# Kernel tuning notes

Measured on AMD Instinct MI355X. Metric: run time of the kernel, lower is better.

The kernel has to match this reference:

```python
import jax, jax.numpy as jnp
import numpy as np
from jax import lax

DN = ('NHWC', 'HWIO', 'NHWC')

def hard_sigmoid(x):
    # Keras ConvLSTM2D default recurrent_activation
    return jnp.clip(0.2 * x + 0.5, 0.0, 1.0)

def conv2d_same(x, w):
    return lax.conv_general_dilated(x, w, (1, 1), 'SAME', dimension_numbers=DN)

def convlstm_layer(x, Wx, Wh, b):
    # x: [B,T,H,W,Cin]; Wx: [kh,kw,Cin,4F]; Wh: [kh,kw,F,4F]; b: [4F]
    B, T, H, W, Cin = x.shape
    F = Wh.shape[2]
    # Precompute input-to-gate convs for all timesteps in one big conv (same math).
    xg = conv2d_same(x.reshape(B * T, H, W, Cin), Wx).reshape(B, T, H, W, 4 * F) + b
    xg = jnp.moveaxis(xg, 1, 0)  # [T,B,H,W,4F]
    h0 = jnp.zeros((B, H, W, F), x.dtype)
    c0 = jnp.zeros((B, H, W, F), x.dtype)

    def step(carry, xg_t):
        h, c = carry
        gates = xg_t + conv2d_same(h, Wh)
        i, f, g, o = jnp.split(gates, 4, axis=-1)
        i = hard_sigmoid(i)
        f = hard_sigmoid(f)
        g = jnp.tanh(g)
        o = hard_sigmoid(o)
        c = f * c + i * g
        h = o * jnp.tanh(c)
        return (h, c), h

    (h, c), hs = lax.scan(step, (h0, c0), xg)
    outputs = jnp.moveaxis(hs, 0, 1)  # [B,T,H,W,F]
    return outputs, h, c

def setup_inputs() -> dict:
    key = jax.random.key(0)
    ks = jax.random.split(key, 8)
    B, T, H, W, Cin = 8, 10, 64, 64, 1
    F = 64
    k = 3
    sc = lambda fan: 1.0 / np.sqrt(fan)
    x = jax.random.normal(ks[0], (B, T, H, W, Cin), jnp.float32)
    Wx0 = jax.random.normal(ks[1], (k, k, Cin, 4 * F), jnp.float32) * sc(k * k * Cin)
    Wh0 = jax.random.normal(ks[2], (k, k, F, 4 * F), jnp.float32) * sc(k * k * F)
    b0 = jax.random.normal(ks[3], (4 * F,), jnp.float32) * 0.01
    Wx1 = jax.random.normal(ks[4], (k, k, F, 4 * F), jnp.float32) * sc(k * k * F)
    Wh1 = jax.random.normal(ks[5], (k, k, F, 4 * F), jnp.float32) * sc(k * k * F)
    b1 = jax.random.normal(ks[6], (4 * F,), jnp.float32) * 0.01
    return {'x': x, 'Wx0': Wx0, 'Wh0': Wh0, 'b0': b0, 'Wx1': Wx1, 'Wh1': Wh1, 'b1': b1}

def reference(x, Wx0, Wh0, b0, Wx1, Wh1, b1):
    out0, h0, c0 = convlstm_layer(x, Wx0, Wh0, b0)
    out1, h1, c1 = convlstm_layer(out0, Wx1, Wh1, b1)
    # Encoder returns per-layer [hidden_state, cell_state]; stack: [L,2,B,H,W,F]
    return jnp.stack([jnp.stack([h0, c0]), jnp.stack([h1, c1])])
```

## Files before the change

### kernel.cpp

```cpp
#include <hip/hip_runtime.h>


typedef __bf16 bf16x8 __attribute__((ext_vector_type(8)));
typedef float f32x4 __attribute__((ext_vector_type(4)));

#define BHWF (8 * 64 * 64 * 64)
#define TSTRIDE 72
#define NCELL 180

__device__ __forceinline__ float hsig(float x) {
    return fminf(fmaxf(fmaf(0.2f, x, 0.5f), 0.0f), 1.0f);
}

__device__ __forceinline__ float ftanh(float x) {
    float e = __expf(2.0f * x);
    return fmaf(-2.0f, __builtin_amdgcn_rcpf(e + 1.0f), 1.0f);
}

__device__ __forceinline__ ushort f2bf(float f) {
    unsigned u = __float_as_uint(f);
    return (ushort)((u + 0x7FFFu + ((u >> 16) & 1u)) >> 16);
}

__global__ void prep_w(const float* __restrict__ s0, const float* __restrict__ s1,
                       const float* __restrict__ s2, const float* __restrict__ wx0,
                       ushort* __restrict__ d0, ushort* __restrict__ d1,
                       ushort* __restrict__ d2, ushort* __restrict__ dx0) {
    int o = blockIdx.x * 256 + threadIdx.x;
    if (blockIdx.y == 3) {
        if (o < 8192) {
            int e    = o & 7;
            int lane = (o >> 3) & 63;
            int g    = (o >> 9) & 3;
            int fq   = (o >> 11) & 3;
            int k = (lane >> 4) * 8 + e;
            int n = g * 64 + fq * 16 + (lane & 15);
            dx0[o] = (k < 9) ? f2bf(wx0[k * 256 + n]) : (ushort)0;
        }
        return;
    }
    const float* s[3] = { s0, s1, s2 };
    ushort* d[3] = { d0, d1, d2 };
    int e    = o & 7;
    int lane = (o >> 3) & 63;
    int g    = (o >> 9) & 3;
    int fq   = (o >> 11) & 3;
    int kc   = (o >> 13) & 1;
    int tap  = o >> 14;
    int n = g * 64 + fq * 16 + (lane & 15);
    int k = tap * 64 + kc * 32 + (lane >> 4) * 8 + e;
    d[blockIdx.y][o] = f2bf(s[blockIdx.y][k * 256 + n]);
}

__device__ __forceinline__ void stage(const ushort* __restrict__ src,
                                      ushort* __restrict__ tile,
                                      int y0, int x0, int tid) {
    for (int v = tid; v < NCELL * 8; v += 256) {
        int cell = v >> 3, j = v & 7;
        int r = cell / 18, cc = cell - r * 18;
        int y = y0 - 1 + r, xx = x0 - 1 + cc;
        uint4 dv = make_uint4(0u, 0u, 0u, 0u);
        if ((unsigned)y < 64u && (unsigned)xx < 64u)
            dv = ((const uint4*)src)[(size_t)((y << 6) + xx) * 8 + j];
        *(uint4*)&tile[cell * TSTRIDE + j * 8] = dv;
    }
}

__device__ __forceinline__ void conv8(const ushort* __restrict__ tile,
                                      const ushort* __restrict__ WS,
                                      f32x4 (&acc)[8][4],
                                      int fq, int lane) {
    const int colA = lane & 15;
    const int quad = (lane >> 4) & 3;
    const ushort* wbase = WS + fq * 2048 + lane * 8;
    #pragma unroll
    for (int kc = 0; kc < 2; ++kc) {
        #pragma unroll
        for (int dx = 0; dx < 3; ++dx) {
            bf16x8 A[10];
            #pragma unroll
            for (int r = 0; r < 10; ++r)
                A[r] = *(const bf16x8*)&tile[(r * 18 + colA + dx) * TSTRIDE + kc * 32 + quad * 8];
            bf16x8 B[3][4];
            {
                const ushort* wp = wbase + (size_t)(dx * 2 + kc) * 8192;
                #pragma unroll
                for (int g = 0; g < 4; ++g) B[0][g] = *(const bf16x8*)&wp[g * 512];
            }
            #pragma unroll
            for (int dy = 0; dy < 3; ++dy) {
                if (dy < 2) {
                    const ushort* wp = wbase + (size_t)(((dy + 1) * 3 + dx) * 2 + kc) * 8192;
                    #pragma unroll
                    for (int g = 0; g < 4; ++g) B[dy + 1][g] = *(const bf16x8*)&wp[g * 512];
                }
                #pragma unroll
                for (int mt = 0; mt < 8; ++mt)
                    #pragma unroll
                    for (int g = 0; g < 4; ++g)
                        acc[mt][g] = __builtin_amdgcn_mfma_f32_16x16x32_bf16(
                            A[mt + dy], B[dy][g], acc[mt][g], 0, 0, 0);
            }
        }
    }
}

__global__ __launch_bounds__(256, 2) void step_merged(
    int l0_active, int l1_active, int last0, int last1,
    const float* __restrict__ x, const ushort* __restrict__ Wx0F,
    const ushort* __restrict__ Wh0S, const float* __restrict__ b0,
    const ushort* __restrict__ h0_prev, float* __restrict__ c0,
    ushort* __restrict__ h0_out, float* __restrict__ oh0, float* __restrict__ oc0,
    const ushort* __restrict__ xin, const ushort* __restrict__ Wx1S,
    const ushort* __restrict__ Wh1S, const float* __restrict__ b1,
    const ushort* __restrict__ h1_prev, float* __restrict__ c1,
    ushort* __restrict__ h1_out, float* __restrict__ oh1, float* __restrict__ oc1)
{
    __shared__ __align__(16) ushort tile1[NCELL * TSTRIDE];
    __shared__ __align__(16) ushort tile2[NCELL * TSTRIDE];
    __shared__ __align__(16) ushort xa[4096];

    const int z = blockIdx.z;
    bool isL1; int b;
    if (l0_active && l1_active) { isL1 = (z >= 8); b = z & 7; }
    else                        { isL1 = (l1_active != 0); b = z; }

    const int tid = threadIdx.x;
    const int lane = tid & 63;
    const int fq = tid >> 6;
    const int colA = lane & 15;
    const int quad = (lane >> 4) & 3;
    const int x0 = blockIdx.x * 16, y0 = blockIdx.y * 8;
    const int f = fq * 16 + colA;

    const ushort* h_prev = isL1 ? h1_prev : h0_prev;
    const float*  bias   = isL1 ? b1 : b0;
    float*        cbuf   = isL1 ? c1 : c0;
    ushort*       hout   = isL1 ? h1_out : h0_out;
    float* hf = isL1 ? (last1 ? oh1 : nullptr) : (last0 ? oh0 : nullptr);
    float* cf = isL1 ? (last1 ? oc1 : nullptr) : (last0 ? oc0 : nullptr);

    if (!isL1) {
        const float* xs = x + (size_t)b * 40960;
        for (int idx = tid; idx < 4096; idx += 256) {
            int e = idx & 7, li = (idx >> 3) & 63, r = idx >> 9;
            int ci = li & 15, qi = li >> 4;
            int k = qi * 8 + e;
            ushort val = 0;
            if (k < 9) {
                int dy = (k * 86) >> 8;
                int dx = k - dy * 3;
                int y = y0 + r + dy - 1, xx = x0 + ci + dx - 1;
                if ((unsigned)y < 64u && (unsigned)xx < 64u)
                    val = f2bf(xs[(y << 6) + xx]);
            }
            xa[idx] = val;
        }
        if (h_prev) stage(h_prev + (size_t)b * 4096 * 64, tile1, y0, x0, tid);
    } else {
        stage(xin + (size_t)b * 4096 * 64, tile1, y0, x0, tid);
        if (h_prev) stage(h_prev + (size_t)b * 4096 * 64, tile2, y0, x0, tid);
    }
    __syncthreads();

    f32x4 acc[8][4];
    #pragma unroll
    for (int g = 0; g < 4; ++g) {
        float bv = bias[g * 64 + f];
        #pragma unroll
        for (int mt = 0; mt < 8; ++mt) {
            acc[mt][g][0] = bv; acc[mt][g][1] = bv;
            acc[mt][g][2] = bv; acc[mt][g][3] = bv;
        }
    }

    if (!isL1) {
        bf16x8 xb[4];
        #pragma unroll
        for (int g = 0; g < 4; ++g)
            xb[g] = *(const bf16x8*)&Wx0F[((fq * 4 + g) * 64 + lane) * 8];
        #pragma unroll
        for (int mt = 0; mt < 8; ++mt) {
            bf16x8 xaf = *(const bf16x8*)&xa[mt * 512 + lane * 8];
            #pragma unroll
            for (int g = 0; g < 4; ++g)
                acc[mt][g] = __builtin_amdgcn_mfma_f32_16x16x32_bf16(
                    xaf, xb[g], acc[mt][g], 0, 0, 0);
        }
        if (h_prev) conv8(tile1, Wh0S, acc, fq, lane);
    } else {
        conv8(tile1, Wx1S, acc, fq, lane);
        if (h_prev) conv8(tile2, Wh1S, acc, fq, lane);
    }

    #pragma unroll
    for (int mt = 0; mt < 8; ++mt) {
        const int y = y0 + mt;
        #pragma unroll
        for (int reg = 0; reg < 4; ++reg) {
            const int xx = x0 + quad * 4 + reg;
            const size_t pidx = ((size_t)b * 4096 + (y << 6) + xx) * 64 + f;
            float cp = h_prev ? cbuf[pidx] : 0.f;
            float iv = hsig(acc[mt][0][reg]);
            float fv = hsig(acc[mt][1][reg]);
            float gv = ftanh(acc[mt][2][reg]);
            float ov = hsig(acc[mt][3][reg]);
            float cn = fmaf(fv, cp, iv * gv);
            float hn = ov * ftanh(cn);
            cbuf[pidx] = cn;
            hout[pidx] = f2bf(hn);
            if (hf) { hf[pidx] = hn; cf[pidx] = cn; }
        }
    }
}

extern "C" void kernel_launch(void* const* d_in, const int* in_sizes, int n_in,
                              void* d_out, int out_size, void* d_ws, size_t ws_size,
                              hipStream_t stream) {
    const float* x   = (const float*)d_in[0];
    const float* Wx0 = (const float*)d_in[1];
    const float* Wh0 = (const float*)d_in[2];
    const float* b0  = (const float*)d_in[3];
    const float* Wx1 = (const float*)d_in[4];
    const float* Wh1 = (const float*)d_in[5];
    const float* b1  = (const float*)d_in[6];
    float* out = (float*)d_out;
    char* ws = (char*)d_ws;

    ushort* h0buf[2] = { (ushort*)ws, (ushort*)(ws + 4u * 1024 * 1024) };
    ushort* h1buf[2] = { (ushort*)(ws + 8u * 1024 * 1024), (ushort*)(ws + 12u * 1024 * 1024) };
    float* c0 = (float*)(ws + 16u * 1024 * 1024);
    float* c1 = (float*)(ws + 24u * 1024 * 1024);
    ushort* Wh0S = (ushort*)(ws + 32u * 1024 * 1024);
    ushort* Wx1S = Wh0S + 147456;
    ushort* Wh1S = Wx1S + 147456;
    ushort* Wx0F = Wh1S + 147456;

    prep_w<<<dim3(576, 4), 256, 0, stream>>>(Wh0, Wx1, Wh1, Wx0,
                                             Wh0S, Wx1S, Wh1S, Wx0F);

    for (int t = 0; t <= 10; ++t) {
        const int has0 = (t < 10), has1 = (t >= 1);
        const int s = t - 1;
        const int tx = has0 ? t : 9;
        dim3 grid(4, 8, (has0 && has1) ? 16 : 8);
        step_merged<<<grid, 256, 0, stream>>>(
            has0, has1, (t == 9), (s == 9),
            x + (size_t)tx * 4096, Wx0F,
            (t >= 1) ? Wh0S : nullptr, b0,
            (t >= 1 && has0) ? h0buf[(t - 1) & 1] : nullptr, c0,
            h0buf[t & 1], out, out + BHWF,
            has1 ? h0buf[s & 1] : nullptr, Wx1S,
            Wh1S, b1,
            (s >= 1) ? h1buf[(s - 1) & 1] : nullptr, c1,
            h1buf[s & 1], out + 2 * (size_t)BHWF, out + 3 * (size_t)BHWF);
    }
}
```

Baseline: 465.8 us.

## Stream conv weights into LDS via async DMA double buffer, reuse single tile

```diff
diff --git a/kernel.cpp b/kernel.cpp
--- a/kernel.cpp
+++ b/kernel.cpp
@@ -66,41 +66,53 @@
     }
 }
 
-__device__ __forceinline__ void conv8(const ushort* __restrict__ tile,
-                                      const ushort* __restrict__ WS,
-                                      f32x4 (&acc)[8][4],
-                                      int fq, int lane) {
+__device__ __forceinline__ void dma4(const ushort* __restrict__ src, ushort* dst) {
+#pragma unroll
+    for (int g = 0; g < 4; ++g)
+        __builtin_amdgcn_global_load_lds(
+            (const __attribute__((address_space(1))) unsigned int*)(src + g * 512),
+            (__attribute__((address_space(3))) unsigned int*)(dst + g * 512),
+            16, 0, 0);
+}
+
+__device__ __forceinline__ void conv_stream(const ushort* __restrict__ tile,
+                                            const ushort* __restrict__ WS,
+                                            ushort* __restrict__ bbuf,
+                                            f32x4 (&acc)[8][4],
+                                            int fq, int lane) {
     const int colA = lane & 15;
     const int quad = (lane >> 4) & 3;
-    const ushort* wbase = WS + fq * 2048 + lane * 8;
-    #pragma unroll
-    for (int kc = 0; kc < 2; ++kc) {
-        #pragma unroll
-        for (int dx = 0; dx < 3; ++dx) {
-            bf16x8 A[10];
-            #pragma unroll
+    const int sl = fq * 2048 + lane * 8;
+    dma4(WS + sl, bbuf + sl);
+    bf16x8 A[10];
+#pragma unroll
+    for (int c = 0; c < 18; ++c) {
+        if (c < 17) {
+            const int c1 = c + 1;
+            const int kc1 = c1 / 9, dx1 = (c1 % 9) / 3, dy1 = c1 % 3;
+            dma4(WS + (size_t)((dy1 * 3 + dx1) * 2 + kc1) * 8192 + sl,
+                 bbuf + (c1 & 1) * 8192 + sl);
+            __asm__ volatile("s_waitcnt vmcnt(4)" ::: "memory");
+        } else {
+            __asm__ volatile("s_waitcnt vmcnt(0)" ::: "memory");
+        }
+        const int kc = c / 9, dx = (c % 9) / 3, dy = c % 3;
+        if (dy == 0) {
+#pragma unroll
             for (int r = 0; r < 10; ++r)
                 A[r] = *(const bf16x8*)&tile[(r * 18 + colA + dx) * TSTRIDE + kc * 32 + quad * 8];
-            bf16x8 B[3][4];
-            {
-                const ushort* wp = wbase + (size_t)(dx * 2 + kc) * 8192;
-                #pragma unroll
-                for (int g = 0; g < 4; ++g) B[0][g] = *(const bf16x8*)&wp[g * 512];
-            }
-            #pragma unroll
-            for (int dy = 0; dy < 3; ++dy) {
-                if (dy < 2) {
-                    const ushort* wp = wbase + (size_t)(((dy + 1) * 3 + dx) * 2 + kc) * 8192;
-                    #pragma unroll
-                    for (int g = 0; g < 4; ++g) B[dy + 1][g] = *(const bf16x8*)&wp[g * 512];
-                }
-                #pragma unroll
-                for (int mt = 0; mt < 8; ++mt)
-                    #pragma unroll
-                    for (int g = 0; g < 4; ++g)
-                        acc[mt][g] = __builtin_amdgcn_mfma_f32_16x16x32_bf16(
-                            A[mt + dy], B[dy][g], acc[mt][g], 0, 0, 0);
-            }
+        }
+        const ushort* bp = bbuf + (c & 1) * 8192 + sl;
+        bf16x8 B0 = *(const bf16x8*)&bp[0];
+        bf16x8 B1 = *(const bf16x8*)&bp[512];
+        bf16x8 B2 = *(const bf16x8*)&bp[1024];
+        bf16x8 B3 = *(const bf16x8*)&bp[1536];
+#pragma unroll
+        for (int mt = 0; mt < 8; ++mt) {
+            acc[mt][0] = __builtin_amdgcn_mfma_f32_16x16x32_bf16(A[mt + dy], B0, acc[mt][0], 0, 0, 0);
+            acc[mt][1] = __builtin_amdgcn_mfma_f32_16x16x32_bf16(A[mt + dy], B1, acc[mt][1], 0, 0, 0);
+            acc[mt][2] = __builtin_amdgcn_mfma_f32_16x16x32_bf16(A[mt + dy], B2, acc[mt][2], 0, 0, 0);
+            acc[mt][3] = __builtin_amdgcn_mfma_f32_16x16x32_bf16(A[mt + dy], B3, acc[mt][3], 0, 0, 0);
         }
     }
 }
@@ -116,8 +128,8 @@
     const ushort* __restrict__ h1_prev, float* __restrict__ c1,
     ushort* __restrict__ h1_out, float* __restrict__ oh1, float* __restrict__ oc1)
 {
-    __shared__ __align__(16) ushort tile1[NCELL * TSTRIDE];
-    __shared__ __align__(16) ushort tile2[NCELL * TSTRIDE];
+    __shared__ __align__(16) ushort tile[NCELL * TSTRIDE];
+    __shared__ __align__(16) ushort bbuf[2 * 8192];
     __shared__ __align__(16) ushort xa[4096];
 
     const int z = blockIdx.z;
@@ -156,18 +168,17 @@
             }
             xa[idx] = val;
         }
-        if (h_prev) stage(h_prev + (size_t)b * 4096 * 64, tile1, y0, x0, tid);
+        if (h_prev) stage(h_prev + (size_t)b * 4096 * 64, tile, y0, x0, tid);
     } else {
-        stage(xin + (size_t)b * 4096 * 64, tile1, y0, x0, tid);
-        if (h_prev) stage(h_prev + (size_t)b * 4096 * 64, tile2, y0, x0, tid);
+        stage(xin + (size_t)b * 4096 * 64, tile, y0, x0, tid);
     }
     __syncthreads();
 
     f32x4 acc[8][4];
-    #pragma unroll
+#pragma unroll
     for (int g = 0; g < 4; ++g) {
         float bv = bias[g * 64 + f];
-        #pragma unroll
+#pragma unroll
         for (int mt = 0; mt < 8; ++mt) {
             acc[mt][g][0] = bv; acc[mt][g][1] = bv;
             acc[mt][g][2] = bv; acc[mt][g][3] = bv;
@@ -176,38 +187,45 @@
 
     if (!isL1) {
         bf16x8 xb[4];
-        #pragma unroll
+#pragma unroll
         for (int g = 0; g < 4; ++g)
             xb[g] = *(const bf16x8*)&Wx0F[((fq * 4 + g) * 64 + lane) * 8];
-        #pragma unroll
+#pragma unroll
         for (int mt = 0; mt < 8; ++mt) {
             bf16x8 xaf = *(const bf16x8*)&xa[mt * 512 + lane * 8];
-            #pragma unroll
+#pragma unroll
             for (int g = 0; g < 4; ++g)
                 acc[mt][g] = __builtin_amdgcn_mfma_f32_16x16x32_bf16(
                     xaf, xb[g], acc[mt][g], 0, 0, 0);
         }
-        if (h_prev) conv8(tile1, Wh0S, acc, fq, lane);
+        if (h_prev) conv_stream(tile, Wh0S, bbuf, acc, fq, lane);
     } else {
-        conv8(tile1, Wx1S, acc, fq, lane);
-        if (h_prev) conv8(tile2, Wh1S, acc, fq, lane);
-    }
-
-    #pragma unroll
+        conv_stream(tile, Wx1S, bbuf, acc, fq, lane);
+        if (h_prev) {
+            __syncthreads();
+            stage(h_prev + (size_t)b * 4096 * 64, tile, y0, x0, tid);
+            __syncthreads();
+            conv_stream(tile, Wh1S, bbuf, acc, fq, lane);
+        }
+    }
+
+#pragma unroll
     for (int mt = 0; mt < 8; ++mt) {
         const int y = y0 + mt;
-        #pragma unroll
+#pragma unroll
         for (int reg = 0; reg < 4; ++reg) {
             const int xx = x0 + quad * 4 + reg;
+            const size_t cidx = ((size_t)((((b * 4 + fq) * 64 + y) * 4 + reg) * 16
+                                 + (x0 >> 2) + quad)) * 16 + colA;
             const size_t pidx = ((size_t)b * 4096 + (y << 6) + xx) * 64 + f;
-            float cp = h_prev ? cbuf[pidx] : 0.f;
+            float cp = h_prev ? cbuf[cidx] : 0.f;
             float iv = hsig(acc[mt][0][reg]);
             float fv = hsig(acc[mt][1][reg]);
             float gv = ftanh(acc[mt][2][reg]);
             float ov = hsig(acc[mt][3][reg]);
             float cn = fmaf(fv, cp, iv * gv);
             float hn = ov * ftanh(cn);
-            cbuf[pidx] = cn;
+            cbuf[cidx] = cn;
             hout[pidx] = f2bf(hn);
             if (hf) { hf[pidx] = hn; cf[pidx] = cn; }
         }
```

Result: faster. 447.5 us (-3.9%).
